# Kernel tuning notes

Hardware: AMD Instinct MI355X
Metric: run time of the kernel (lower is better)

Reference implementation:

```python
import jax, jax.numpy as jnp
import numpy as np

N_NODES = 100000
N_EDGES = 1600000
D_FEAT = 64
ORDER = 2


def setup_inputs() -> dict:
    key = jax.random.key(0)
    k1, k2, k3, k4 = jax.random.split(key, 4)
    x = jax.random.normal(k1, (N_NODES, D_FEAT), dtype=jnp.float32)
    edge_row = jnp.sort(jax.random.randint(k2, (N_EDGES,), 0, N_NODES, dtype=jnp.int32))
    edge_col = jax.random.randint(k3, (N_EDGES,), 0, N_NODES, dtype=jnp.int32)
    # positive edge weights ~ normalized adjacency values
    edge_val = jax.random.uniform(k4, (N_EDGES,), dtype=jnp.float32)
    return {"x": x, "edge_row": edge_row, "edge_col": edge_col, "edge_val": edge_val}


def reference(x, edge_row, edge_col, edge_val):
    # SGConvolution: x <- adj @ x, repeated `order` times (no trainable params).
    # adj is sparse COO: adj[edge_row[e], edge_col[e]] = edge_val[e].
    def spmm(h):
        # gather source features, scale by edge weight, scatter-add to rows
        msg = edge_val[:, None] * h[edge_col]          # [E, D]
        return jax.ops.segment_sum(msg, edge_row, num_segments=N_NODES)  # [N, D]

    h = x
    for _ in range(ORDER):
        h = spmm(h)
    return h
```

## Files before the change

### kernel.cpp

```cpp
#include <hip/hip_runtime.h>
#include <hip/hip_fp16.h>


#define N_NODES 100000
#define N_EDGES 1600000
#define D_FEAT  64
#define ROWS    4

__device__ __forceinline__ float readlane_f(float x, int j) {
    return __uint_as_float(__builtin_amdgcn_readlane(__float_as_uint(x), j));
}

__device__ __forceinline__ void store_feat(__half* p, float v) { *p = __float2half_rn(v); }
__device__ __forceinline__ void store_feat(float*  p, float v) { *p = v; }

__global__ __launch_bounds__(256) void prep_kernel(
    const float* __restrict__ x, __half* __restrict__ h16,
    const int* __restrict__ erow, int* __restrict__ rowptr)
{
    const int gid = blockIdx.x * blockDim.x + threadIdx.x;
    const int n4  = (N_NODES * D_FEAT) / 4;
    if (gid < n4) {
        const float4 v = ((const float4*)x)[gid];
        ((__half2*)h16)[2 * gid]     = __floats2half2_rn(v.x, v.y);
        ((__half2*)h16)[2 * gid + 1] = __floats2half2_rn(v.z, v.w);
    } else {
        const int n = gid - n4;
        if (n <= N_NODES) {
            int lo = 0, hi = N_EDGES;
            while (lo < hi) {
                const int mid = (lo + hi) >> 1;
                if (erow[mid] < n) lo = mid + 1; else hi = mid;
            }
            rowptr[n] = lo;
        }
    }
}

template <typename OutT>
__global__ __launch_bounds__(256) void sg_spmm_csr(
    const __half* __restrict__ h,
    const int*    __restrict__ rowptr,
    const int*    __restrict__ ecol,
    const float*  __restrict__ eval,
    OutT*         __restrict__ out)
{
    const int lane = threadIdx.x & 63;
    const int wave = (int)((blockIdx.x * blockDim.x + threadIdx.x) >> 6);
    const int r0   = wave * ROWS;
    if (r0 >= N_NODES) return;

    const int rp0 = __builtin_amdgcn_readfirstlane(rowptr[r0 + 0]);
    const int rp1 = __builtin_amdgcn_readfirstlane(rowptr[r0 + 1]);
    const int rp2 = __builtin_amdgcn_readfirstlane(rowptr[r0 + 2]);
    const int rp3 = __builtin_amdgcn_readfirstlane(rowptr[r0 + 3]);
    const int rp4 = __builtin_amdgcn_readfirstlane(rowptr[r0 + 4]);

    float acc = 0.0f;
    int   r   = 0;
    int   bnd = rp1;

    for (int eb = rp0; eb < rp4; eb += 64) {
        const int n = min(64, rp4 - eb);
        const int   c_v = (lane < n) ? ecol[eb + lane] : 0;
        const float w_v = (lane < n) ? eval[eb + lane] : 0.0f;

        __half g[2][16];
#pragma unroll
        for (int j = 0; j < 16; ++j) {
            const int c = __builtin_amdgcn_readlane(c_v, j);
            g[0][j] = h[(size_t)c * D_FEAT + lane];
        }
#pragma unroll
        for (int k = 0; k < 4; ++k) {
            if (k * 16 < n) {
                if ((k + 1) * 16 < n) {
#pragma unroll
                    for (int j = 0; j < 16; ++j) {
                        const int c = __builtin_amdgcn_readlane(c_v, (k + 1) * 16 + j);
                        g[(k + 1) & 1][j] = h[(size_t)c * D_FEAT + lane];
                    }
                }
#pragma unroll
                for (int j = 0; j < 16; ++j) {
                    const int e = eb + k * 16 + j;
                    while (r < ROWS && e >= bnd) {
                        store_feat(&out[(size_t)(r0 + r) * D_FEAT + lane], acc);
                        acc = 0.0f;
                        ++r;
                        bnd = (r == 1) ? rp2 : (r == 2) ? rp3 : rp4;
                    }
                    acc += readlane_f(w_v, k * 16 + j) * __half2float(g[k & 1][j]);
                }
            }
        }
    }
    while (r < ROWS) {
        store_feat(&out[(size_t)(r0 + r) * D_FEAT + lane], acc);
        acc = 0.0f;
        ++r;
    }
}

__global__ __launch_bounds__(256) void spmm_atomic_f32(
    const float* __restrict__ h, const int* __restrict__ erow,
    const int* __restrict__ ecol, const float* __restrict__ eval,
    float* __restrict__ out)
{
    const int lane  = threadIdx.x & 63;
    const int wave  = (int)((blockIdx.x * blockDim.x + threadIdx.x) >> 6);
    const int start = wave * 64;
    if (start >= N_EDGES) return;
    int cur_row = erow[start];
    float acc = 0.0f;
    for (int e = start; e < start + 64; ++e) {
        const int r = erow[e];
        if (r != cur_row) {
            atomicAdd(&out[(size_t)cur_row * D_FEAT + lane], acc);
            acc = 0.0f; cur_row = r;
        }
        acc += eval[e] * h[(size_t)ecol[e] * D_FEAT + lane];
    }
    atomicAdd(&out[(size_t)cur_row * D_FEAT + lane], acc);
}

extern "C" void kernel_launch(void* const* d_in, const int* in_sizes, int n_in,
                              void* d_out, int out_size, void* d_ws, size_t ws_size,
                              hipStream_t stream) {
    const float* x    = (const float*)d_in[0];
    const int*   erow = (const int*)  d_in[1];
    const int*   ecol = (const int*)  d_in[2];
    const float* eval = (const float*)d_in[3];
    float*       out  = (float*)d_out;

    const size_t n_elem    = (size_t)N_NODES * D_FEAT;
    const size_t f16_bytes = n_elem * sizeof(__half);
    const size_t off_a     = 1 << 20;
    const size_t off_b     = off_a + f16_bytes;
    const size_t needed    = off_b + f16_bytes;

    const int threads = 256;

    if (ws_size >= needed) {
        int*    rowptr = (int*)d_ws;
        __half* h16a   = (__half*)((char*)d_ws + off_a);
        __half* h16b   = (__half*)((char*)d_ws + off_b);

        const int prep_total  = (int)(n_elem / 4) + N_NODES + 1;
        const int prep_blocks = (prep_total + threads - 1) / threads;
        const int spmm_blocks = (N_NODES / ROWS) * 64 / threads;

        prep_kernel<<<prep_blocks, threads, 0, stream>>>(x, h16a, erow, rowptr);
        sg_spmm_csr<__half><<<spmm_blocks, threads, 0, stream>>>(
            h16a, rowptr, ecol, eval, h16b);
        sg_spmm_csr<float><<<spmm_blocks, threads, 0, stream>>>(
            h16b, rowptr, ecol, eval, out);
    } else {
        float* h1 = (float*)d_ws;
        const size_t f32_bytes = n_elem * sizeof(float);
        hipMemsetAsync(h1, 0, f32_bytes, stream);
        hipMemsetAsync(out, 0, f32_bytes, stream);
        const int blocks = (N_EDGES / 64) * 64 / threads;
        spmm_atomic_f32<<<blocks, threads, 0, stream>>>(x, erow, ecol, eval, h1);
        spmm_atomic_f32<<<blocks, threads, 0, stream>>>(h1, erow, ecol, eval, out);
    }
}
```

Measured before the change: 173.3 us.

## Gather two edges per wave using half2 loads split across half-waves

Each wave now processes two edges per step: the lower 32 lanes load one neighbor row and the upper 32 lanes another, each lane reading a half2 (two features). Partial sums are combined with a cross-half shuffle when a row is flushed, and stores become paired half2/float2 writes from the lower half only. Column and weight indices for the next 64-edge chunk are also prefetched one iteration ahead. This halves the number of gather instructions and widens each load, at the cost of extra shuffles, more complex boundary handling for row changes between paired edges, and idle upper lanes during stores.

```diff
diff --git a/kernel.cpp b/kernel.cpp
--- a/kernel.cpp
+++ b/kernel.cpp
@@ -11,8 +11,13 @@
     return __uint_as_float(__builtin_amdgcn_readlane(__float_as_uint(x), j));
 }
 
-__device__ __forceinline__ void store_feat(__half* p, float v) { *p = __float2half_rn(v); }
-__device__ __forceinline__ void store_feat(float*  p, float v) { *p = v; }
+__device__ __forceinline__ void store_pair(__half* row, int j, float x, float y) {
+    ((__half2*)row)[j] = __floats2half2_rn(x, y);
+}
+__device__ __forceinline__ void store_pair(float* row, int j, float x, float y) {
+    float2 v; v.x = x; v.y = y;
+    ((float2*)row)[j] = v;
+}
 
 __global__ __launch_bounds__(256) void prep_kernel(
     const float* __restrict__ x, __half* __restrict__ h16,
@@ -45,9 +50,11 @@
     const float*  __restrict__ eval,
     OutT*         __restrict__ out)
 {
-    const int lane = threadIdx.x & 63;
-    const int wave = (int)((blockIdx.x * blockDim.x + threadIdx.x) >> 6);
-    const int r0   = wave * ROWS;
+    const int  lane   = threadIdx.x & 63;
+    const int  lane31 = lane & 31;
+    const bool hi     = lane >= 32;
+    const int  wave   = (int)((blockIdx.x * blockDim.x + threadIdx.x) >> 6);
+    const int  r0     = wave * ROWS;
     if (r0 >= N_NODES) return;
 
     const int rp0 = __builtin_amdgcn_readfirstlane(rowptr[r0 + 0]);
@@ -56,50 +63,85 @@
     const int rp3 = __builtin_amdgcn_readfirstlane(rowptr[r0 + 3]);
     const int rp4 = __builtin_amdgcn_readfirstlane(rowptr[r0 + 4]);
 
-    float acc = 0.0f;
-    int   r   = 0;
-    int   bnd = rp1;
+    float accx = 0.0f, accy = 0.0f;
+    int   r    = 0;
+    int   bnd  = rp1;
+
+#define FLUSH_ROW()                                                         \
+    do {                                                                    \
+        float tx = accx + __shfl_xor(accx, 32, 64);                         \
+        float ty = accy + __shfl_xor(accy, 32, 64);                         \
+        if (!hi) store_pair(out + (size_t)(r0 + r) * D_FEAT, lane31, tx, ty);\
+        accx = 0.0f; accy = 0.0f;                                           \
+        ++r;                                                                \
+        bnd = (r == 1) ? rp2 : (r == 2) ? rp3 : rp4;                        \
+    } while (0)
+
+    int cv = 0; float wv = 0.0f;
+    if (rp0 < rp4) {
+        const int n0 = rp4 - rp0;
+        cv = (lane < n0) ? ecol[rp0 + lane] : 0;
+        wv = (lane < n0) ? eval[rp0 + lane] : 0.0f;
+    }
 
     for (int eb = rp0; eb < rp4; eb += 64) {
         const int n = min(64, rp4 - eb);
-        const int   c_v = (lane < n) ? ecol[eb + lane] : 0;
-        const float w_v = (lane < n) ? eval[eb + lane] : 0.0f;
-
-        __half g[2][16];
-#pragma unroll
-        for (int j = 0; j < 16; ++j) {
-            const int c = __builtin_amdgcn_readlane(c_v, j);
-            g[0][j] = h[(size_t)c * D_FEAT + lane];
+
+        int cvn = 0; float wvn = 0.0f;
+        if (eb + 64 < rp4) {
+            const int nn = min(64, rp4 - (eb + 64));
+            cvn = (lane < nn) ? ecol[eb + 64 + lane] : 0;
+            wvn = (lane < nn) ? eval[eb + 64 + lane] : 0.0f;
+        }
+
+        __half2 g[2][8];
+#pragma unroll
+        for (int j = 0; j < 8; ++j) {
+            const int c0  = __builtin_amdgcn_readlane(cv, 2 * j);
+            const int c1  = __builtin_amdgcn_readlane(cv, 2 * j + 1);
+            const int col = hi ? c1 : c0;
+            g[0][j] = ((const __half2*)(h + (size_t)col * D_FEAT))[lane31];
         }
 #pragma unroll
         for (int k = 0; k < 4; ++k) {
             if (k * 16 < n) {
                 if ((k + 1) * 16 < n) {
 #pragma unroll
-                    for (int j = 0; j < 16; ++j) {
-                        const int c = __builtin_amdgcn_readlane(c_v, (k + 1) * 16 + j);
-                        g[(k + 1) & 1][j] = h[(size_t)c * D_FEAT + lane];
+                    for (int j = 0; j < 8; ++j) {
+                        const int p   = (k + 1) * 8 + j;
+                        const int c0  = __builtin_amdgcn_readlane(cv, 2 * p);
+                        const int c1  = __builtin_amdgcn_readlane(cv, 2 * p + 1);
+                        const int col = hi ? c1 : c0;
+                        g[(k + 1) & 1][j] = ((const __half2*)(h + (size_t)col * D_FEAT))[lane31];
                     }
                 }
 #pragma unroll
-                for (int j = 0; j < 16; ++j) {
-                    const int e = eb + k * 16 + j;
-                    while (r < ROWS && e >= bnd) {
-                        store_feat(&out[(size_t)(r0 + r) * D_FEAT + lane], acc);
-                        acc = 0.0f;
-                        ++r;
-                        bnd = (r == 1) ? rp2 : (r == 2) ? rp3 : rp4;
+                for (int j = 0; j < 8; ++j) {
+                    const int   p   = k * 8 + j;
+                    const int   E0  = eb + 2 * p;
+                    const int   E1  = E0 + 1;
+                    const float sw0 = readlane_f(wv, 2 * p);
+                    const float sw1 = readlane_f(wv, 2 * p + 1);
+                    const float2 f  = __half22float2(g[k & 1][j]);
+
+                    while (r < ROWS && E0 >= bnd) FLUSH_ROW();
+                    if (E1 >= bnd && r < ROWS) {
+                        const float wl = hi ? 0.0f : sw0;
+                        accx += wl * f.x; accy += wl * f.y;
+                        while (r < ROWS && E1 >= bnd) FLUSH_ROW();
+                        const float wh = hi ? sw1 : 0.0f;
+                        accx += wh * f.x; accy += wh * f.y;
+                    } else {
+                        const float ws = hi ? sw1 : sw0;
+                        accx += ws * f.x; accy += ws * f.y;
                     }
-                    acc += readlane_f(w_v, k * 16 + j) * __half2float(g[k & 1][j]);
                 }
             }
         }
-    }
-    while (r < ROWS) {
-        store_feat(&out[(size_t)(r0 + r) * D_FEAT + lane], acc);
-        acc = 0.0f;
-        ++r;
-    }
+        cv = cvn; wv = wvn;
+    }
+    while (r < ROWS) FLUSH_ROW();
+#undef FLUSH_ROW
 }
 
 __global__ __launch_bounds__(256) void spmm_atomic_f32(
```

Result: no change. 171.6 us (-1.0%).
